# Optimization experiments

Measured on AMD Instinct MI355X. Metric: run time of the kernel, lower is better.

The kernel has to match this reference:

```python
import jax, jax.numpy as jnp
import numpy as np

DIM = 1024
HEADS = 16
HEAD_DIM = DIM // HEADS
BS, SQ, SK = 4, 2048, 2048


def setup_inputs() -> dict:
    key = jax.random.key(0)
    ks = jax.random.split(key, 12)
    s = 1.0 / np.sqrt(DIM)
    return {
        "x_q": jax.random.normal(ks[0], (BS, SQ, DIM), jnp.float32),
        "x_k": jax.random.normal(ks[1], (BS, SK, DIM), jnp.float32),
        "x_v": jax.random.normal(ks[2], (BS, SK, DIM), jnp.float32),
        "mask": jax.random.randint(ks[3], (BS, SQ, SK), 0, 2, jnp.int32),
        # torch nn.Linear weights: [out, in]; y = x @ W.T + b
        "wq": jax.random.uniform(ks[4], (DIM, DIM), jnp.float32, -s, s),
        "bq": jax.random.uniform(ks[5], (DIM,), jnp.float32, -s, s),
        "wk": jax.random.uniform(ks[6], (DIM, DIM), jnp.float32, -s, s),
        "bk": jax.random.uniform(ks[7], (DIM,), jnp.float32, -s, s),
        "wv": jax.random.uniform(ks[8], (DIM, DIM), jnp.float32, -s, s),
        "bv": jax.random.uniform(ks[9], (DIM,), jnp.float32, -s, s),
        "wo": jax.random.uniform(ks[10], (DIM, DIM), jnp.float32, -s, s),
        "bo": jax.random.uniform(ks[11], (DIM,), jnp.float32, -s, s),
    }


def reference(x_q, x_k, x_v, mask, wq, bq, wk, bk, wv, bv, wo, bo):
    bs, sq, dim = x_q.shape
    q = x_q @ wq.T + bq
    k = x_k @ wk.T + bk
    v = x_v @ wv.T + bv
    # [b, h, s, d]
    qh = q.reshape(bs, sq, HEADS, HEAD_DIM).transpose(0, 2, 1, 3)
    kh = k.reshape(bs, -1, HEADS, HEAD_DIM).transpose(0, 2, 1, 3)
    vh = v.reshape(bs, -1, HEADS, HEAD_DIM).transpose(0, 2, 1, 3)
    scale = 1.0 / np.sqrt(HEAD_DIM).astype(np.float32)
    s = jnp.einsum("bhqd,bhkd->bhqk", qh, kh) * scale
    # mask==0 positions set to -10000 across all heads
    s = jnp.where(mask[:, None, :, :] == 0, jnp.float32(-10000.0), s)
    p = jax.nn.softmax(s, axis=-1)
    z = jnp.einsum("bhqk,bhkd->bhqd", p, vh)
    z = z.transpose(0, 2, 1, 3).reshape(bs, sq, dim)
    return z @ wo.T + bo
```

## Files before the change

kernel.cpp:

```cpp
#include <hip/hip_runtime.h>

#define DEVINL __device__ __forceinline__

typedef _Float16 half8 __attribute__((ext_vector_type(8)));
typedef _Float16 half4 __attribute__((ext_vector_type(4)));
typedef __fp16 fp16x2 __attribute__((ext_vector_type(2)));
typedef float f32x4 __attribute__((ext_vector_type(4)));
typedef float float4v __attribute__((ext_vector_type(4)));

static constexpr int kDIM = 1024;
static constexpr int kHEADS = 16;
static constexpr int kHD = 64;
static constexpr int kBS = 4;
static constexpr int kSQ = 2048;
static constexpr int kSK = 2048;
static constexpr int kMTOT = kBS * kSQ;

DEVINL void async_copy16(void* lds, const void* g) {
  __builtin_amdgcn_global_load_lds(
      (__attribute__((address_space(1))) unsigned int*)(g),
      (__attribute__((address_space(3))) unsigned int*)(lds), 16, 0, 0);
}

DEVINL unsigned pkrtz_u32(float a, float b) {
  fp16x2 h = __builtin_amdgcn_cvt_pkrtz(a, b);
  unsigned u;
  __builtin_memcpy(&u, &h, 4);
  return u;
}

__global__ void prep_kernel(const int* __restrict__ mask,
                            unsigned* __restrict__ bits,
                            const float* __restrict__ s0, const float* __restrict__ s1,
                            const float* __restrict__ s2, const float* __restrict__ s3,
                            _Float16* __restrict__ d0, _Float16* __restrict__ d1,
                            _Float16* __restrict__ d2, _Float16* __restrict__ d3) {
  int bid = blockIdx.x;
  if (bid < 2048) {
    int t = bid * 256 + threadIdx.x;
    const int4* p = (const int4*)(mask + (size_t)t * 32);
    unsigned w = 0;
#pragma unroll
    for (int j = 0; j < 8; ++j) {
      int4 v = p[j];
      w |= (v.x != 0 ? 1u : 0u) << (j * 4);
      w |= (v.y != 0 ? 1u : 0u) << (j * 4 + 1);
      w |= (v.z != 0 ? 1u : 0u) << (j * 4 + 2);
      w |= (v.w != 0 ? 1u : 0u) << (j * 4 + 3);
    }
    bits[t] = w;
  } else {
    int cb = bid - 2048;
    int which = cb >> 9;
    const float* s = which == 0 ? s0 : which == 1 ? s1 : which == 2 ? s2 : s3;
    _Float16* d = which == 0 ? d0 : which == 1 ? d1 : which == 2 ? d2 : d3;
    int j = ((cb & 511) * 256 + threadIdx.x) * 8;
    float4v a0 = *(const float4v*)(s + j);
    float4v a1 = *(const float4v*)(s + j + 4);
    half8 h;
    h[0] = (_Float16)a0[0]; h[1] = (_Float16)a0[1];
    h[2] = (_Float16)a0[2]; h[3] = (_Float16)a0[3];
    h[4] = (_Float16)a1[0]; h[5] = (_Float16)a1[1];
    h[6] = (_Float16)a1[2]; h[7] = (_Float16)a1[3];
    *(half8*)(d + j) = h;
  }
}

template <bool A_F32, bool OUT_F16>
DEVINL void gemm_body(const void* __restrict__ Aptr,
                      const _Float16* __restrict__ B,
                      const float* __restrict__ bias,
                      void* __restrict__ Cptr, int N, int K, int bid,
                      _Float16* As, _Float16* Bs) {
  const int tid = threadIdx.x;
  const int lane = tid & 63;
  const int w = tid >> 6;
  const int wr = w >> 1, wc = w & 1;
  const int bm0 = (bid & 63) << 7;
  const int bn0 = (bid >> 6) << 7;
  const int c16 = lane & 15;
  const int hi4 = lane >> 4;

  f32x4 acc[4][4] = {};

  for (int k0 = 0; k0 < K; k0 += 64) {
    __syncthreads();
    if (A_F32) {
      const float* A32 = (const float*)Aptr;
#pragma unroll
      for (int i = 0; i < 4; ++i) {
        int c = i * 256 + tid;
        int row = c >> 3, seg = c & 7;
        int gseg = seg ^ (row & 7);
        const float* src = A32 + (size_t)(bm0 + row) * K + k0 + gseg * 8;
        float4v a0 = *(const float4v*)src;
        float4v a1 = *(const float4v*)(src + 4);
        half8 h;
        h[0] = (_Float16)a0[0]; h[1] = (_Float16)a0[1];
        h[2] = (_Float16)a0[2]; h[3] = (_Float16)a0[3];
        h[4] = (_Float16)a1[0]; h[5] = (_Float16)a1[1];
        h[6] = (_Float16)a1[2]; h[7] = (_Float16)a1[3];
        *(half8*)((char*)As + c * 16) = h;
      }
    } else {
      const _Float16* A16 = (const _Float16*)Aptr;
#pragma unroll
      for (int i = 0; i < 4; ++i) {
        int c = i * 256 + tid;
        int row = c >> 3, seg = c & 7;
        int gseg = seg ^ (row & 7);
        async_copy16((char*)As + i * 4096 + w * 1024,
                     A16 + (size_t)(bm0 + row) * K + k0 + gseg * 8);
      }
    }
#pragma unroll
    for (int i = 0; i < 4; ++i) {
      int c = i * 256 + tid;
      int row = c >> 3, seg = c & 7;
      int gseg = seg ^ (row & 7);
      async_copy16((char*)Bs + i * 4096 + w * 1024,
                   B + (size_t)(bn0 + row) * K + k0 + gseg * 8);
    }
    __syncthreads();
#pragma unroll
    for (int kf = 0; kf < 2; ++kf) {
      half8 af[4], bf[4];
#pragma unroll
      for (int m = 0; m < 4; ++m) {
        int row = wr * 64 + m * 16 + c16;
        int off = row * 128 + (((kf * 4 + hi4) << 4) ^ ((row & 7) << 4));
        af[m] = *(const half8*)((const char*)As + off);
      }
#pragma unroll
      for (int n = 0; n < 4; ++n) {
        int row = wc * 64 + n * 16 + c16;
        int off = row * 128 + (((kf * 4 + hi4) << 4) ^ ((row & 7) << 4));
        bf[n] = *(const half8*)((const char*)Bs + off);
      }
#pragma unroll
      for (int m = 0; m < 4; ++m)
#pragma unroll
        for (int n = 0; n < 4; ++n)
          acc[m][n] =
              __builtin_amdgcn_mfma_f32_16x16x32_f16(af[m], bf[n], acc[m][n], 0, 0, 0);
    }
  }
#pragma unroll
  for (int n = 0; n < 4; ++n) {
    int col = bn0 + wc * 64 + n * 16 + c16;
    float bv = bias[col];
#pragma unroll
    for (int m = 0; m < 4; ++m) {
      int row0 = bm0 + wr * 64 + m * 16 + (hi4 << 2);
#pragma unroll
      for (int r = 0; r < 4; ++r) {
        float v = acc[m][n][r] + bv;
        if (OUT_F16)
          ((_Float16*)Cptr)[(size_t)(row0 + r) * N + col] = (_Float16)v;
        else
          ((float*)Cptr)[(size_t)(row0 + r) * N + col] = v;
      }
    }
  }
}

__launch_bounds__(256, 2)
__global__ void gemm_qkv_kernel(const float* __restrict__ xq,
                                const float* __restrict__ xk,
                                const float* __restrict__ xv,
                                const _Float16* __restrict__ Wq,
                                const _Float16* __restrict__ Wk,
                                const _Float16* __restrict__ Wv,
                                const float* __restrict__ bq,
                                const float* __restrict__ bk,
                                const float* __restrict__ bv,
                                _Float16* __restrict__ Q16,
                                _Float16* __restrict__ K16,
                                _Float16* __restrict__ V16) {
  __shared__ __align__(16) _Float16 As[128 * 64];
  __shared__ __align__(16) _Float16 Bs[128 * 64];
  int which = blockIdx.x >> 9;
  int bid = blockIdx.x & 511;
  const float* A = which == 0 ? xq : which == 1 ? xk : xv;
  const _Float16* B = which == 0 ? Wq : which == 1 ? Wk : Wv;
  const float* bias = which == 0 ? bq : which == 1 ? bk : bv;
  _Float16* C = which == 0 ? Q16 : which == 1 ? K16 : V16;
  gemm_body<true, true>(A, B, bias, C, kDIM, kDIM, bid, As, Bs);
}

__launch_bounds__(256, 2)
__global__ void gemm_o_kernel(const _Float16* __restrict__ Z16,
                              const _Float16* __restrict__ Wo,
                              const float* __restrict__ bo,
                              float* __restrict__ out) {
  __shared__ __align__(16) _Float16 As[128 * 64];
  __shared__ __align__(16) _Float16 Bs[128 * 64];
  gemm_body<false, false>(Z16, Wo, bo, out, kDIM, kDIM, blockIdx.x, As, Bs);
}

__global__ void transpose_v_kernel(const _Float16* __restrict__ V,
                                   _Float16* __restrict__ Vt) {
  __shared__ _Float16 tile[64][72];
  int bid = blockIdx.x;
  int bh = bid & 63;
  int b = bh >> 4, h = bh & 15;
  int s0 = (bid >> 6) * 64;
  int tid = threadIdx.x;
  {
    int s = tid >> 2, dseg = tid & 3;
    const half8* src =
        (const half8*)(V + (size_t)(b * kSK + s0 + s) * kDIM + h * 64 + dseg * 16);
    half8 v0 = src[0], v1 = src[1];
#pragma unroll
    for (int j = 0; j < 8; ++j) {
      tile[s][dseg * 16 + j] = v0[j];
      tile[s][dseg * 16 + 8 + j] = v1[j];
    }
  }
  __syncthreads();
  {
    int d = tid >> 2, sseg = tid & 3;
    half8 o0, o1;
#pragma unroll
    for (int j = 0; j < 8; ++j) {
      o0[j] = tile[sseg * 16 + j][d];
      o1[j] = tile[sseg * 16 + 8 + j][d];
    }
    half8* dst = (half8*)(Vt + ((size_t)(bh * 64 + d)) * kSK + s0 + sseg * 16);
    dst[0] = o0;
    dst[1] = o1;
  }
}

__launch_bounds__(256, 3)
__global__ void attn_kernel(const _Float16* __restrict__ Q,
                            const _Float16* __restrict__ K,
                            const _Float16* __restrict__ Vt,
                            const unsigned* __restrict__ maskbits,
                            _Float16* __restrict__ Z) {
  __shared__ __align__(16) char smem[32768 + 128 * 72 * 2];
  _Float16* Ps = (_Float16*)(smem + 32768);
  const int tid = threadIdx.x, lane = tid & 63, w = tid >> 6;
  const int bid = blockIdx.x;
  const int hb = bid & 63;
  const int b = hb >> 4, h = hb & 15;
  const int qt0 = (bid >> 6) * 128;
  const int c16 = lane & 15;
  const int hi4 = lane >> 4;
  const int row4 = hi4 << 2;
  const unsigned* mb = maskbits + (size_t)b * kSQ * (kSK / 32);

#pragma unroll
  for (int i = 0; i < 4; ++i) {
    int c = i * 256 + tid;
    int row = c >> 3, seg = c & 7;
    int gseg = seg ^ (row & 7);
    async_copy16(smem + i * 4096 + w * 1024,
                 Q + (size_t)(b * kSQ + qt0 + row) * kDIM + h * 64 + gseg * 8);
  }
  __syncthreads();
  half8 qf[2][2];
#pragma unroll
  for (int m = 0; m < 2; ++m)
#pragma unroll
    for (int kf = 0; kf < 2; ++kf) {
      int row = w * 32 + m * 16 + c16;
      int off = row * 128 + (((kf * 4 + hi4) << 4) ^ ((row & 7) << 4));
      qf[m][kf] = *(const half8*)(smem + off);
      qf[m][kf] *= (_Float16)0.18033688f;
    }
  __syncthreads();

  auto stage_kv = [&](int bufoff, int ktt) {
#pragma unroll
    for (int i = 0; i < 2; ++i) {
      int c = i * 256 + tid;
      int row = c >> 3, seg = c & 7;
      int gseg = seg ^ (row & 7);
      async_copy16(smem + bufoff + i * 4096 + w * 1024,
                   K + (size_t)(b * kSK + ktt + row) * kDIM + h * 64 + gseg * 8);
    }
#pragma unroll
    for (int i = 0; i < 2; ++i) {
      int c = i * 256 + tid;
      int row = c >> 3, seg = c & 7;
      int gseg = seg ^ (row & 7);
      async_copy16(smem + bufoff + 8192 + i * 4096 + w * 1024,
                   Vt + (size_t)((b * kHEADS + h) * kHD + row) * kSK + ktt + gseg * 8);
    }
  };

  unsigned long long mq_cur[2], mq_nxt[2];
  stage_kv(0, 0);
#pragma unroll
  for (int m2 = 0; m2 < 2; ++m2) {
    int q = qt0 + w * 32 + m2 * 16 + c16;
    mq_cur[m2] = *(const unsigned long long*)(mb + (size_t)q * (kSK / 32));
  }
  asm volatile("s_waitcnt vmcnt(0)" ::: "memory");
  __builtin_amdgcn_s_barrier();
  asm volatile("" ::: "memory");

  f32x4 zacc[2][4] = {};
  f32x4 lacc[2] = {};
  half8 ones8;
#pragma unroll
  for (int j = 0; j < 8; ++j) ones8[j] = (_Float16)1.0f;

  int cur = 0;
  for (int kt = 0; kt < kSK; kt += 64) {
    if (kt + 64 < kSK) {
      stage_kv((cur ^ 1) * 16384, kt + 64);
#pragma unroll
      for (int m2 = 0; m2 < 2; ++m2) {
        int q = qt0 + w * 32 + m2 * 16 + c16;
        mq_nxt[m2] = *(const unsigned long long*)(mb + (size_t)q * (kSK / 32) +
                                                  ((kt + 64) >> 5));
      }
    }
    const char* bufK = smem + cur * 16384;
    const char* bufV = bufK + 8192;

    f32x4 s[2][4] = {};
    __builtin_amdgcn_s_setprio(1);
#pragma unroll
    for (int kf = 0; kf < 2; ++kf)
#pragma unroll
      for (int n = 0; n < 4; ++n) {
        int key = n * 16 + c16;
        half8 kb = *(const half8*)(bufK + key * 128 +
                                   (((kf * 4 + hi4) << 4) ^ ((key & 7) << 4)));
        s[0][n] = __builtin_amdgcn_mfma_f32_16x16x32_f16(kb, qf[0][kf], s[0][n], 0, 0, 0);
        s[1][n] = __builtin_amdgcn_mfma_f32_16x16x32_f16(kb, qf[1][kf], s[1][n], 0, 0, 0);
      }
    __builtin_amdgcn_s_setprio(0);

#pragma unroll
    for (int m2 = 0; m2 < 2; ++m2) {
      unsigned lo = (unsigned)(mq_cur[m2] >> (hi4 * 4));
      unsigned hh = (unsigned)(mq_cur[m2] >> (hi4 * 4 + 32));
      int q_local = w * 32 + m2 * 16 + c16;
#pragma unroll
      for (int n = 0; n < 4; ++n) {
        unsigned sel = (n < 2) ? lo : hh;
        const int base = (n & 1) * 16;
        float p[4];
#pragma unroll
        for (int r = 0; r < 4; ++r) {
          float pv = __builtin_exp2f(s[m2][n][r]);
          int msk = __builtin_amdgcn_sbfe((int)sel, base + r, 1);
          pv = __uint_as_float(__float_as_uint(pv) & (unsigned)msk);
          p[r] = pv;
        }
        uint2 pw = {pkrtz_u32(p[0], p[1]), pkrtz_u32(p[2], p[3])};
        *(uint2*)((char*)Ps + q_local * 144 + n * 32 + hi4 * 8) = pw;
      }
    }

    __builtin_amdgcn_s_setprio(1);
#pragma unroll
    for (int kf2 = 0; kf2 < 2; ++kf2) {
      half8 vb[4];
#pragma unroll
      for (int df = 0; df < 4; ++df) {
        int d = df * 16 + c16;
        vb[df] = *(const half8*)(bufV + d * 128 +
                                 (((kf2 * 4 + hi4) << 4) ^ ((d & 7) << 4)));
      }
#pragma unroll
      for (int m2 = 0; m2 < 2; ++m2) {
        int q_local = w * 32 + m2 * 16 + c16;
        half8 pa = *(const half8*)((char*)Ps + q_local * 144 + (kf2 * 4 + hi4) * 16);
        lacc[m2] = __builtin_amdgcn_mfma_f32_16x16x32_f16(pa, ones8, lacc[m2], 0, 0, 0);
#pragma unroll
        for (int df = 0; df < 4; ++df)
          zacc[m2][df] =
              __builtin_amdgcn_mfma_f32_16x16x32_f16(pa, vb[df], zacc[m2][df], 0, 0, 0);
      }
    }
    __builtin_amdgcn_s_setprio(0);

    asm volatile("s_waitcnt vmcnt(0)" ::: "memory");
    __builtin_amdgcn_s_barrier();
    asm volatile("" ::: "memory");
    mq_cur[0] = mq_nxt[0];
    mq_cur[1] = mq_nxt[1];
    cur ^= 1;
  }

#pragma unroll
  for (int m2 = 0; m2 < 2; ++m2)
#pragma unroll
    for (int r = 0; r < 4; ++r) {
      float inv = 1.0f / lacc[m2][r];
      int q = qt0 + w * 32 + m2 * 16 + row4 + r;
#pragma unroll
      for (int df = 0; df < 4; ++df) {
        int d = df * 16 + c16;
        Z[(size_t)(b * kSQ + q) * kDIM + h * 64 + d] =
            (_Float16)(zacc[m2][df][r] * inv);
      }
    }
}

extern "C" void kernel_launch(void* const* d_in, const int* in_sizes, int n_in,
                              void* d_out, int out_size, void* d_ws,
                              size_t ws_size, hipStream_t stream) {
  const float* x_q = (const float*)d_in[0];
  const float* x_k = (const float*)d_in[1];
  const float* x_v = (const float*)d_in[2];
  const int* mask = (const int*)d_in[3];
  const float* wq = (const float*)d_in[4];
  const float* bq = (const float*)d_in[5];
  const float* wk = (const float*)d_in[6];
  const float* bk = (const float*)d_in[7];
  const float* wv = (const float*)d_in[8];
  const float* bv = (const float*)d_in[9];
  const float* wo = (const float*)d_in[10];
  const float* bo = (const float*)d_in[11];

  const size_t W_ELEMS = (size_t)1024 * 1024;
  const size_t T_ELEMS = (size_t)kMTOT * kDIM;
  const size_t NEED = (4 * W_ELEMS + 5 * T_ELEMS) * 2 + (size_t)kBS * kSQ * (kSK / 32) * 4;
  if (ws_size < NEED) return;

  char* ws = (char*)d_ws;
  _Float16* Wq16 = (_Float16*)ws;
  _Float16* Wk16 = Wq16 + W_ELEMS;
  _Float16* Wv16 = Wk16 + W_ELEMS;
  _Float16* Wo16 = Wv16 + W_ELEMS;
  _Float16* Q16 = Wo16 + W_ELEMS;
  _Float16* K16 = Q16 + T_ELEMS;
  _Float16* V16 = K16 + T_ELEMS;
  _Float16* Vt16 = V16 + T_ELEMS;
  _Float16* Z16 = Vt16 + T_ELEMS;
  unsigned* mbits = (unsigned*)(Z16 + T_ELEMS);

  prep_kernel<<<4096, 256, 0, stream>>>(mask, mbits, wq, wk, wv, wo,
                                        Wq16, Wk16, Wv16, Wo16);

  gemm_qkv_kernel<<<1536, 256, 0, stream>>>(x_q, x_k, x_v, Wq16, Wk16, Wv16,
                                            bq, bk, bv, Q16, K16, V16);

  transpose_v_kernel<<<2048, 256, 0, stream>>>(V16, Vt16);

  attn_kernel<<<1024, 256, 0, stream>>>(Q16, K16, Vt16, mbits, Z16);

  gemm_o_kernel<<<512, 256, 0, stream>>>(Z16, Wo16, bo, (float*)d_out);
}
```

Before: 257.0 us.

## Double attention query tile to 256 rows per block for K/V reuse

Each attention block now handles 256 query rows instead of 128, with each wave owning 64 rows (four 16-row MFMA groups). The goal is to halve global K/V staging and LDS K/V reads per query, since each staged K/V tile now feeds twice as many MFMAs. The P scratch buffer stays the same size and is reused for two row-pair passes per wave. In exchange the grid halves to 512 blocks, launch bounds drop to 2 blocks per SIMD, and register pressure rises, which may hurt latency hiding and CU load balance.

```diff
diff --git a/kernel.cpp b/kernel.cpp
--- a/kernel.cpp
+++ b/kernel.cpp
@@ -232,26 +232,26 @@
   }
 }
 
-__launch_bounds__(256, 3)
+__launch_bounds__(256, 2)
 __global__ void attn_kernel(const _Float16* __restrict__ Q,
                             const _Float16* __restrict__ K,
                             const _Float16* __restrict__ Vt,
                             const unsigned* __restrict__ maskbits,
                             _Float16* __restrict__ Z) {
-  __shared__ __align__(16) char smem[32768 + 128 * 72 * 2];
-  _Float16* Ps = (_Float16*)(smem + 32768);
+  __shared__ __align__(16) char smem[32768 + 128 * 144];
+  char* Ps = smem + 32768;
   const int tid = threadIdx.x, lane = tid & 63, w = tid >> 6;
   const int bid = blockIdx.x;
   const int hb = bid & 63;
   const int b = hb >> 4, h = hb & 15;
-  const int qt0 = (bid >> 6) * 128;
+  const int qt0 = (bid >> 6) * 256;
   const int c16 = lane & 15;
   const int hi4 = lane >> 4;
   const int row4 = hi4 << 2;
   const unsigned* mb = maskbits + (size_t)b * kSQ * (kSK / 32);
 
 #pragma unroll
-  for (int i = 0; i < 4; ++i) {
+  for (int i = 0; i < 8; ++i) {
     int c = i * 256 + tid;
     int row = c >> 3, seg = c & 7;
     int gseg = seg ^ (row & 7);
@@ -259,15 +259,15 @@
                  Q + (size_t)(b * kSQ + qt0 + row) * kDIM + h * 64 + gseg * 8);
   }
   __syncthreads();
-  half8 qf[2][2];
-#pragma unroll
-  for (int m = 0; m < 2; ++m)
+  half8 qf[4][2];
+#pragma unroll
+  for (int m2 = 0; m2 < 4; ++m2)
 #pragma unroll
     for (int kf = 0; kf < 2; ++kf) {
-      int row = w * 32 + m * 16 + c16;
+      int row = w * 64 + m2 * 16 + c16;
       int off = row * 128 + (((kf * 4 + hi4) << 4) ^ ((row & 7) << 4));
-      qf[m][kf] = *(const half8*)(smem + off);
-      qf[m][kf] *= (_Float16)0.18033688f;
+      qf[m2][kf] = *(const half8*)(smem + off);
+      qf[m2][kf] *= (_Float16)0.18033688f;
     }
   __syncthreads();
 
@@ -290,19 +290,19 @@
     }
   };
 
-  unsigned long long mq_cur[2], mq_nxt[2];
+  unsigned long long mq_cur[4], mq_nxt[4];
   stage_kv(0, 0);
 #pragma unroll
-  for (int m2 = 0; m2 < 2; ++m2) {
-    int q = qt0 + w * 32 + m2 * 16 + c16;
+  for (int m2 = 0; m2 < 4; ++m2) {
+    int q = qt0 + w * 64 + m2 * 16 + c16;
     mq_cur[m2] = *(const unsigned long long*)(mb + (size_t)q * (kSK / 32));
   }
   asm volatile("s_waitcnt vmcnt(0)" ::: "memory");
   __builtin_amdgcn_s_barrier();
   asm volatile("" ::: "memory");
 
-  f32x4 zacc[2][4] = {};
-  f32x4 lacc[2] = {};
+  f32x4 zacc[4][4] = {};
+  f32x4 lacc[4] = {};
   half8 ones8;
 #pragma unroll
   for (int j = 0; j < 8; ++j) ones8[j] = (_Float16)1.0f;
@@ -312,8 +312,8 @@
     if (kt + 64 < kSK) {
       stage_kv((cur ^ 1) * 16384, kt + 64);
 #pragma unroll
-      for (int m2 = 0; m2 < 2; ++m2) {
-        int q = qt0 + w * 32 + m2 * 16 + c16;
+      for (int m2 = 0; m2 < 4; ++m2) {
+        int q = qt0 + w * 64 + m2 * 16 + c16;
         mq_nxt[m2] = *(const unsigned long long*)(mb + (size_t)q * (kSK / 32) +
                                                   ((kt + 64) >> 5));
       }
@@ -321,7 +321,7 @@
     const char* bufK = smem + cur * 16384;
     const char* bufV = bufK + 8192;
 
-    f32x4 s[2][4] = {};
+    f32x4 s[4][4] = {};
     __builtin_amdgcn_s_setprio(1);
 #pragma unroll
     for (int kf = 0; kf < 2; ++kf)
@@ -330,70 +330,75 @@
         int key = n * 16 + c16;
         half8 kb = *(const half8*)(bufK + key * 128 +
                                    (((kf * 4 + hi4) << 4) ^ ((key & 7) << 4)));
-        s[0][n] = __builtin_amdgcn_mfma_f32_16x16x32_f16(kb, qf[0][kf], s[0][n], 0, 0, 0);
-        s[1][n] = __builtin_amdgcn_mfma_f32_16x16x32_f16(kb, qf[1][kf], s[1][n], 0, 0, 0);
+#pragma unroll
+        for (int m2 = 0; m2 < 4; ++m2)
+          s[m2][n] = __builtin_amdgcn_mfma_f32_16x16x32_f16(kb, qf[m2][kf], s[m2][n], 0, 0, 0);
       }
     __builtin_amdgcn_s_setprio(0);
 
 #pragma unroll
-    for (int m2 = 0; m2 < 2; ++m2) {
-      unsigned lo = (unsigned)(mq_cur[m2] >> (hi4 * 4));
-      unsigned hh = (unsigned)(mq_cur[m2] >> (hi4 * 4 + 32));
-      int q_local = w * 32 + m2 * 16 + c16;
-#pragma unroll
-      for (int n = 0; n < 4; ++n) {
-        unsigned sel = (n < 2) ? lo : hh;
-        const int base = (n & 1) * 16;
-        float p[4];
-#pragma unroll
-        for (int r = 0; r < 4; ++r) {
-          float pv = __builtin_exp2f(s[m2][n][r]);
-          int msk = __builtin_amdgcn_sbfe((int)sel, base + r, 1);
-          pv = __uint_as_float(__float_as_uint(pv) & (unsigned)msk);
-          p[r] = pv;
+    for (int p = 0; p < 2; ++p) {
+#pragma unroll
+      for (int mi = 0; mi < 2; ++mi) {
+        const int m2 = p * 2 + mi;
+        unsigned lo = (unsigned)(mq_cur[m2] >> (hi4 * 4));
+        unsigned hh = (unsigned)(mq_cur[m2] >> (hi4 * 4 + 32));
+        int q_ps = w * 32 + mi * 16 + c16;
+#pragma unroll
+        for (int n = 0; n < 4; ++n) {
+          unsigned sel = (n < 2) ? lo : hh;
+          const int base = (n & 1) * 16;
+          float pp[4];
+#pragma unroll
+          for (int r = 0; r < 4; ++r) {
+            float pv = __builtin_exp2f(s[m2][n][r]);
+            int msk = __builtin_amdgcn_sbfe((int)sel, base + r, 1);
+            pv = __uint_as_float(__float_as_uint(pv) & (unsigned)msk);
+            pp[r] = pv;
+          }
+          uint2 pw = {pkrtz_u32(pp[0], pp[1]), pkrtz_u32(pp[2], pp[3])};
+          *(uint2*)(Ps + q_ps * 144 + n * 32 + hi4 * 8) = pw;
         }
-        uint2 pw = {pkrtz_u32(p[0], p[1]), pkrtz_u32(p[2], p[3])};
-        *(uint2*)((char*)Ps + q_local * 144 + n * 32 + hi4 * 8) = pw;
-      }
-    }
-
-    __builtin_amdgcn_s_setprio(1);
-#pragma unroll
-    for (int kf2 = 0; kf2 < 2; ++kf2) {
-      half8 vb[4];
-#pragma unroll
-      for (int df = 0; df < 4; ++df) {
-        int d = df * 16 + c16;
-        vb[df] = *(const half8*)(bufV + d * 128 +
-                                 (((kf2 * 4 + hi4) << 4) ^ ((d & 7) << 4)));
-      }
-#pragma unroll
-      for (int m2 = 0; m2 < 2; ++m2) {
-        int q_local = w * 32 + m2 * 16 + c16;
-        half8 pa = *(const half8*)((char*)Ps + q_local * 144 + (kf2 * 4 + hi4) * 16);
-        lacc[m2] = __builtin_amdgcn_mfma_f32_16x16x32_f16(pa, ones8, lacc[m2], 0, 0, 0);
-#pragma unroll
-        for (int df = 0; df < 4; ++df)
-          zacc[m2][df] =
-              __builtin_amdgcn_mfma_f32_16x16x32_f16(pa, vb[df], zacc[m2][df], 0, 0, 0);
-      }
-    }
-    __builtin_amdgcn_s_setprio(0);
+      }
+      __builtin_amdgcn_s_setprio(1);
+#pragma unroll
+      for (int kf2 = 0; kf2 < 2; ++kf2) {
+        half8 vb[4];
+#pragma unroll
+        for (int df = 0; df < 4; ++df) {
+          int d = df * 16 + c16;
+          vb[df] = *(const half8*)(bufV + d * 128 +
+                                   (((kf2 * 4 + hi4) << 4) ^ ((d & 7) << 4)));
+        }
+#pragma unroll
+        for (int mi = 0; mi < 2; ++mi) {
+          const int m2 = p * 2 + mi;
+          int q_ps = w * 32 + mi * 16 + c16;
+          half8 pa = *(const half8*)(Ps + q_ps * 144 + (kf2 * 4 + hi4) * 16);
+          lacc[m2] = __builtin_amdgcn_mfma_f32_16x16x32_f16(pa, ones8, lacc[m2], 0, 0, 0);
+#pragma unroll
+          for (int df = 0; df < 4; ++df)
+            zacc[m2][df] =
+                __builtin_amdgcn_mfma_f32_16x16x32_f16(pa, vb[df], zacc[m2][df], 0, 0, 0);
+        }
+      }
+      __builtin_amdgcn_s_setprio(0);
+    }
 
     asm volatile("s_waitcnt vmcnt(0)" ::: "memory");
     __builtin_amdgcn_s_barrier();
     asm volatile("" ::: "memory");
-    mq_cur[0] = mq_nxt[0];
-    mq_cur[1] = mq_nxt[1];
+#pragma unroll
+    for (int m2 = 0; m2 < 4; ++m2) mq_cur[m2] = mq_nxt[m2];
     cur ^= 1;
   }
 
 #pragma unroll
-  for (int m2 = 0; m2 < 2; ++m2)
+  for (int m2 = 0; m2 < 4; ++m2)
 #pragma unroll
     for (int r = 0; r < 4; ++r) {
       float inv = 1.0f / lacc[m2][r];
-      int q = qt0 + w * 32 + m2 * 16 + row4 + r;
+      int q = qt0 + w * 64 + m2 * 16 + row4 + r;
 #pragma unroll
       for (int df = 0; df < 4; ++df) {
         int d = df * 16 + c16;
@@ -444,7 +449,7 @@
 
   transpose_v_kernel<<<2048, 256, 0, stream>>>(V16, Vt16);
 
-  attn_kernel<<<1024, 256, 0, stream>>>(Q16, K16, Vt16, mbits, Z16);
+  attn_kernel<<<512, 256, 0, stream>>>(Q16, K16, Vt16, mbits, Z16);
 
   gemm_o_kernel<<<512, 256, 0, stream>>>(Z16, Wo16, bo, (float*)d_out);
 }
```

New measurement: 256.0 us. No clear change (-0.4%).
